# Kernel optimization log

Measured on AMD Instinct MI355X. Metric: run time of the kernel, lower is better.

The kernel has to match this reference:

```python
import jax, jax.numpy as jnp
import numpy as np

NUM_NODES = 50000
FEAT_DIM = 64
HIDDEN = 128
OUT_DIM = 128
NUM_EDGES = 640000


def setup_inputs() -> dict:
    key = jax.random.key(0)
    ks = jax.random.split(key, 8)
    edge_index = jax.random.randint(ks[0], (2, NUM_EDGES), 0, NUM_NODES, dtype=jnp.int32)
    emb = jax.random.normal(ks[1], (NUM_NODES, FEAT_DIM), dtype=jnp.float32) * 0.1
    # SAGEConv: lin_l (aggregated neighbors, with bias) and lin_r (root, no bias)
    s1 = 1.0 / np.sqrt(FEAT_DIM)
    W1l = jax.random.uniform(ks[2], (HIDDEN, FEAT_DIM), jnp.float32, -s1, s1)
    b1l = jnp.zeros((HIDDEN,), jnp.float32)
    W1r = jax.random.uniform(ks[3], (HIDDEN, FEAT_DIM), jnp.float32, -s1, s1)
    s2 = 1.0 / np.sqrt(HIDDEN)
    W2l = jax.random.uniform(ks[4], (OUT_DIM, HIDDEN), jnp.float32, -s2, s2)
    b2l = jnp.zeros((OUT_DIM,), jnp.float32)
    W2r = jax.random.uniform(ks[5], (OUT_DIM, HIDDEN), jnp.float32, -s2, s2)
    return {"edge_index": edge_index, "emb": emb, "W1l": W1l, "b1l": b1l,
            "W1r": W1r, "W2l": W2l, "b2l": b2l, "W2r": W2r}


def _sage_conv(x, src, dst, Wl, bl, Wr):
    # mean-aggregate source features at target nodes, then two linear paths
    msg = x[src]                                   # [E, d]
    agg = jax.ops.segment_sum(msg, dst, num_segments=NUM_NODES)
    deg = jax.ops.segment_sum(jnp.ones((src.shape[0],), x.dtype), dst,
                              num_segments=NUM_NODES)
    mean = agg / jnp.maximum(deg, 1.0)[:, None]    # [N, d]
    return mean @ Wl.T + bl + x @ Wr.T             # [N, out]


def reference(edge_index, emb, W1l, b1l, W1r, W2l, b2l, W2r):
    src, dst = edge_index[0], edge_index[1]
    h = jax.nn.relu(_sage_conv(emb, src, dst, W1l, b1l, W1r))
    return _sage_conv(h, src, dst, W2l, b2l, W2r)
```

## Files before the change

### kernel.cpp

```cpp
#include <hip/hip_runtime.h>

#define N_NODES 50000
#define FEAT    64
#define HID     128
#define N_EDGES 640000
#define NBLK    196
#define GCAP    64
#define SSTR    68

typedef __attribute__((ext_vector_type(8))) short bf16x8;
typedef __attribute__((ext_vector_type(4))) float f32x4;

static __device__ __forceinline__ unsigned short f2bf(float f) {
    unsigned u = __float_as_uint(f);
    u = u + 0x7fffu + ((u >> 16) & 1u);
    return (unsigned short)(u >> 16);
}
static __device__ __forceinline__ float bflo(unsigned u) {
    return __uint_as_float(u << 16);
}
static __device__ __forceinline__ float bfhi(unsigned u) {
    return __uint_as_float(u & 0xffff0000u);
}

static __device__ __forceinline__ void gridbar(int* bar, int gen) {
    __syncthreads();
    if (threadIdx.x == 0) {
        __threadfence();
        int arrived = atomicAdd(&bar[0], 1);
        if (arrived == NBLK - 1) {
            atomicExch(&bar[0], 0);
            __threadfence();
            atomicExch(&bar[1], gen);
        } else {
            while (atomicAdd(&bar[1], 0) < gen) __builtin_amdgcn_s_sleep(2);
        }
        __threadfence();
    }
    __syncthreads();
}

__global__ __launch_bounds__(256) void histcvt_kernel(
        const int* __restrict__ dst, const float* __restrict__ emb,
        const float* __restrict__ W1l, const float* __restrict__ W1r,
        const float* __restrict__ W2l, const float* __restrict__ W2r,
        int* __restrict__ count, int* __restrict__ eslot,
        unsigned* __restrict__ emb_bf_u, unsigned* __restrict__ Wbf_u) {
    int gtid = blockIdx.x * 256 + threadIdx.x;
    if (gtid < N_EDGES) {
        int slot = atomicAdd(&count[dst[gtid]], 1);
        eslot[gtid] = slot;
    }
    for (int i = gtid; i < N_NODES * FEAT / 2; i += N_EDGES) {
        float2 v = ((const float2*)emb)[i];
        emb_bf_u[i] = ((unsigned)f2bf(v.y) << 16) | (unsigned)f2bf(v.x);
    }
    if (gtid < 24576) {
        int w = gtid * 2;
        float lo, hi;
        if (w < 8192)       { lo = W1l[w];         hi = W1l[w + 1]; }
        else if (w < 16384) { lo = W1r[w - 8192];  hi = W1r[w - 8191]; }
        else if (w < 32768) { lo = W2l[w - 16384]; hi = W2l[w - 16383]; }
        else                { lo = W2r[w - 32768]; hi = W2r[w - 32767]; }
        Wbf_u[gtid] = ((unsigned)f2bf(hi) << 16) | (unsigned)f2bf(lo);
    }
}

__global__ __launch_bounds__(256) void scanperm_kernel(
        const int* __restrict__ count, int* offset, int* dhist, int* dcur,
        int* bsum, int* boff, int* dstart, int* perm, int* bar) {
    __shared__ int tmp[256];
    __shared__ int lh[64];
    __shared__ int lb2[64];
    int t = threadIdx.x;
    int gtid = blockIdx.x * 256 + t;

    {
        if (t < 64) lh[t] = 0;
        int v = (gtid < N_NODES) ? count[gtid] : 0;
        tmp[t] = v;
        __syncthreads();
        if (gtid < N_NODES) atomicAdd(&lh[v < 63 ? v : 63], 1);
        for (int off = 1; off < 256; off <<= 1) {
            int add = (t >= off) ? tmp[t - off] : 0;
            __syncthreads();
            tmp[t] += add;
            __syncthreads();
        }
        if (gtid < N_NODES) offset[gtid] = tmp[t] - v;
        if (t == 255) bsum[blockIdx.x] = tmp[255];
        if (t < 64 && lh[t] > 0) atomicAdd(&dhist[t], lh[t]);
    }
    gridbar(bar, 1);

    if (blockIdx.x < 2) {
        const int* in  = (blockIdx.x == 0) ? bsum : dhist;
        int*       out = (blockIdx.x == 0) ? boff : dstart;
        int cnt        = (blockIdx.x == 0) ? NBLK : 64;
        int v = (t < cnt) ? in[t] : 0;
        tmp[t] = v;
        __syncthreads();
        for (int off = 1; off < 256; off <<= 1) {
            int add = (t >= off) ? tmp[t - off] : 0;
            __syncthreads();
            tmp[t] += add;
            __syncthreads();
        }
        if (t < cnt) out[t] = tmp[t] - v;
    }
    gridbar(bar, 2);

    if (gtid < N_NODES) offset[gtid] += boff[blockIdx.x];
    if (gtid == 0) offset[N_NODES] = N_EDGES;
    {
        if (t < 64) lh[t] = 0;
        __syncthreads();
        int d = 0, slot = 0;
        if (gtid < N_NODES) {
            int c = count[gtid];
            d = c < 63 ? c : 63;
            slot = atomicAdd(&lh[d], 1);
        }
        __syncthreads();
        if (t < 64 && lh[t] > 0) lb2[t] = atomicAdd(&dcur[t], lh[t]);
        __syncthreads();
        if (gtid < N_NODES) perm[dstart[d] + lb2[d] + slot] = gtid;
    }
}

__global__ void fill_kernel(const int* __restrict__ src, const int* __restrict__ dst,
                            const int* __restrict__ offset,
                            const int* __restrict__ eslot, int* __restrict__ esrc) {
    int e = blockIdx.x * blockDim.x + threadIdx.x;
    if (e >= N_EDGES) return;
    esrc[offset[dst[e]] + eslot[e]] = src[e];
}

__global__ __launch_bounds__(256, 4) void fgemm1_kernel(
        const unsigned short* __restrict__ embb, const int* __restrict__ offset,
        const int* __restrict__ esrc, const int* __restrict__ perm,
        const short* __restrict__ Wl, const short* __restrict__ Wr,
        const float* __restrict__ bias, unsigned short* __restrict__ hout) {
    __shared__ unsigned short smean[16][72];
    __shared__ int sidx[16][SSTR];
    __shared__ int nid[16];
    int t = threadIdx.x;
    int bid = (int)gridDim.x - 1 - (int)blockIdx.x;
    if (t < 16) nid[t] = perm[bid * 16 + t];
    __syncthreads();

    int sub = t >> 4, fl = t & 15;
    int n = nid[sub];
    int beg = offset[n], deg = offset[n + 1] - beg;
    bool fast = deg <= GCAP;
    if (fast) { for (int j = fl; j < deg; j += 16) sidx[sub][j] = esrc[beg + j]; }
    float A0[4] = {0,0,0,0}, A1[4] = {0,0,0,0};
    const uint2* eb2 = (const uint2*)embb;
    #define ACC2(A, v) { \
        A[0]+=bflo((v).x); A[1]+=bfhi((v).x); A[2]+=bflo((v).y); A[3]+=bfhi((v).y); }
    {
        int i = 0;
        if (fast) {
            for (; i + 8 <= deg; i += 8) {
                int4 i0 = *(const int4*)&sidx[sub][i];
                int4 i1 = *(const int4*)&sidx[sub][i + 4];
                uint2 r0 = eb2[(size_t)i0.x * 16 + fl];
                uint2 r1 = eb2[(size_t)i0.y * 16 + fl];
                uint2 r2 = eb2[(size_t)i0.z * 16 + fl];
                uint2 r3 = eb2[(size_t)i0.w * 16 + fl];
                uint2 r4 = eb2[(size_t)i1.x * 16 + fl];
                uint2 r5 = eb2[(size_t)i1.y * 16 + fl];
                uint2 r6 = eb2[(size_t)i1.z * 16 + fl];
                uint2 r7 = eb2[(size_t)i1.w * 16 + fl];
                ACC2(A0, r0) ACC2(A1, r1) ACC2(A0, r2) ACC2(A1, r3)
                ACC2(A0, r4) ACC2(A1, r5) ACC2(A0, r6) ACC2(A1, r7)
            }
            for (; i + 4 <= deg; i += 4) {
                int4 i0 = *(const int4*)&sidx[sub][i];
                uint2 r0 = eb2[(size_t)i0.x * 16 + fl];
                uint2 r1 = eb2[(size_t)i0.y * 16 + fl];
                uint2 r2 = eb2[(size_t)i0.z * 16 + fl];
                uint2 r3 = eb2[(size_t)i0.w * 16 + fl];
                ACC2(A0, r0) ACC2(A1, r1) ACC2(A0, r2) ACC2(A1, r3)
            }
            for (; i < deg; ++i) {
                uint2 v = eb2[(size_t)sidx[sub][i] * 16 + fl];
                ACC2(A0, v)
            }
        } else {
            for (; i < deg; ++i) {
                uint2 v = eb2[(size_t)esrc[beg + i] * 16 + fl];
                ACC2(A0, v)
            }
        }
    }
    #undef ACC2
    float dinv = 1.0f / fmaxf((float)deg, 1.0f);
    float s0 = (A0[0] + A1[0]) * dinv;
    float s1 = (A0[1] + A1[1]) * dinv;
    float s2 = (A0[2] + A1[2]) * dinv;
    float s3 = (A0[3] + A1[3]) * dinv;
    uint2 o;
    o.x = ((unsigned)f2bf(s1) << 16) | (unsigned)f2bf(s0);
    o.y = ((unsigned)f2bf(s3) << 16) | (unsigned)f2bf(s2);
    *(uint2*)&smean[sub][fl * 4] = o;
    __syncthreads();

    int wave = t >> 6, lane = t & 63;
    int col = lane & 15, quad = lane >> 4;
    int ncol = nid[col];
    int nt0 = wave * 2, nt1 = nt0 + 1;
    f32x4 acc0 = (f32x4){0.f,0.f,0.f,0.f}, acc1 = (f32x4){0.f,0.f,0.f,0.f};
    #pragma unroll
    for (int kb = 0; kb < FEAT; kb += 32) {
        bf16x8 am = *(const bf16x8*)&smean[col][kb + quad * 8];
        bf16x8 ax = *(const bf16x8*)(embb + (size_t)ncol * FEAT + kb + quad * 8);
        bf16x8 bl0 = *(const bf16x8*)(Wl + (nt0 * 16 + col) * FEAT + kb + quad * 8);
        bf16x8 br0 = *(const bf16x8*)(Wr + (nt0 * 16 + col) * FEAT + kb + quad * 8);
        bf16x8 bl1 = *(const bf16x8*)(Wl + (nt1 * 16 + col) * FEAT + kb + quad * 8);
        bf16x8 br1 = *(const bf16x8*)(Wr + (nt1 * 16 + col) * FEAT + kb + quad * 8);
        acc0 = __builtin_amdgcn_mfma_f32_16x16x32_bf16(am, bl0, acc0, 0, 0, 0);
        acc0 = __builtin_amdgcn_mfma_f32_16x16x32_bf16(ax, br0, acc0, 0, 0, 0);
        acc1 = __builtin_amdgcn_mfma_f32_16x16x32_bf16(am, bl1, acc1, 0, 0, 0);
        acc1 = __builtin_amdgcn_mfma_f32_16x16x32_bf16(ax, br1, acc1, 0, 0, 0);
    }
    float bv0 = bias[nt0 * 16 + col];
    float bv1 = bias[nt1 * 16 + col];
    #pragma unroll
    for (int r = 0; r < 4; ++r) {
        int node = nid[quad * 4 + r];
        hout[(size_t)node * HID + nt0 * 16 + col] = f2bf(fmaxf(acc0[r] + bv0, 0.f));
        hout[(size_t)node * HID + nt1 * 16 + col] = f2bf(fmaxf(acc1[r] + bv1, 0.f));
    }
}

__global__ __launch_bounds__(256, 4) void fgemm2_kernel(
        const unsigned short* __restrict__ hbf, const int* __restrict__ offset,
        const int* __restrict__ esrc, const int* __restrict__ perm,
        const short* __restrict__ Wl, const short* __restrict__ Wr,
        const float* __restrict__ bias, float* __restrict__ out) {
    __shared__ unsigned short smean[16][136];
    __shared__ int sidx[16][SSTR];
    __shared__ int nid[16];
    int t = threadIdx.x;
    int bid = (int)gridDim.x - 1 - (int)blockIdx.x;
    if (t < 16) nid[t] = perm[bid * 16 + t];
    __syncthreads();

    int sub = t >> 4, fl = t & 15;
    int n = nid[sub];
    int beg = offset[n], deg = offset[n + 1] - beg;
    bool fast = deg <= GCAP;
    if (fast) { for (int j = fl; j < deg; j += 16) sidx[sub][j] = esrc[beg + j]; }
    float A0[8] = {0,0,0,0,0,0,0,0}, A1[8] = {0,0,0,0,0,0,0,0};
    const uint4* hb4 = (const uint4*)hbf;
    #define ACCU(A, v) { \
        A[0]+=bflo((v).x); A[1]+=bfhi((v).x); A[2]+=bflo((v).y); A[3]+=bfhi((v).y); \
        A[4]+=bflo((v).z); A[5]+=bfhi((v).z); A[6]+=bflo((v).w); A[7]+=bfhi((v).w); }
    {
        int i = 0;
        if (fast) {
            for (; i + 8 <= deg; i += 8) {
                int4 i0 = *(const int4*)&sidx[sub][i];
                int4 i1 = *(const int4*)&sidx[sub][i + 4];
                uint4 r0 = hb4[(size_t)i0.x * 16 + fl];
                uint4 r1 = hb4[(size_t)i0.y * 16 + fl];
                uint4 r2 = hb4[(size_t)i0.z * 16 + fl];
                uint4 r3 = hb4[(size_t)i0.w * 16 + fl];
                uint4 r4 = hb4[(size_t)i1.x * 16 + fl];
                uint4 r5 = hb4[(size_t)i1.y * 16 + fl];
                uint4 r6 = hb4[(size_t)i1.z * 16 + fl];
                uint4 r7 = hb4[(size_t)i1.w * 16 + fl];
                ACCU(A0, r0) ACCU(A1, r1) ACCU(A0, r2) ACCU(A1, r3)
                ACCU(A0, r4) ACCU(A1, r5) ACCU(A0, r6) ACCU(A1, r7)
            }
            for (; i + 4 <= deg; i += 4) {
                int4 i0 = *(const int4*)&sidx[sub][i];
                uint4 r0 = hb4[(size_t)i0.x * 16 + fl];
                uint4 r1 = hb4[(size_t)i0.y * 16 + fl];
                uint4 r2 = hb4[(size_t)i0.z * 16 + fl];
                uint4 r3 = hb4[(size_t)i0.w * 16 + fl];
                ACCU(A0, r0) ACCU(A1, r1) ACCU(A0, r2) ACCU(A1, r3)
            }
            for (; i < deg; ++i) {
                uint4 v = hb4[(size_t)sidx[sub][i] * 16 + fl];
                ACCU(A0, v)
            }
        } else {
            for (; i < deg; ++i) {
                uint4 v = hb4[(size_t)esrc[beg + i] * 16 + fl];
                ACCU(A0, v)
            }
        }
    }
    #undef ACCU
    float dinv = 1.0f / fmaxf((float)deg, 1.0f);
    unsigned ow[4];
    #pragma unroll
    for (int k = 0; k < 4; ++k) {
        float lo = (A0[2*k]   + A1[2*k])   * dinv;
        float hi = (A0[2*k+1] + A1[2*k+1]) * dinv;
        ow[k] = ((unsigned)f2bf(hi) << 16) | (unsigned)f2bf(lo);
    }
    uint4 o4 = {ow[0], ow[1], ow[2], ow[3]};
    *(uint4*)&smean[sub][fl * 8] = o4;
    __syncthreads();

    int wave = t >> 6, lane = t & 63;
    int col = lane & 15, quad = lane >> 4;
    int ncol = nid[col];
    int nt0 = wave * 2, nt1 = nt0 + 1;
    f32x4 acc0 = (f32x4){0.f,0.f,0.f,0.f}, acc1 = (f32x4){0.f,0.f,0.f,0.f};
    #pragma unroll
    for (int kb = 0; kb < HID; kb += 32) {
        bf16x8 am = *(const bf16x8*)&smean[col][kb + quad * 8];
        bf16x8 ax = *(const bf16x8*)(hbf + (size_t)ncol * HID + kb + quad * 8);
        bf16x8 bl0 = *(const bf16x8*)(Wl + (nt0 * 16 + col) * HID + kb + quad * 8);
        bf16x8 br0 = *(const bf16x8*)(Wr + (nt0 * 16 + col) * HID + kb + quad * 8);
        bf16x8 bl1 = *(const bf16x8*)(Wl + (nt1 * 16 + col) * HID + kb + quad * 8);
        bf16x8 br1 = *(const bf16x8*)(Wr + (nt1 * 16 + col) * HID + kb + quad * 8);
        acc0 = __builtin_amdgcn_mfma_f32_16x16x32_bf16(am, bl0, acc0, 0, 0, 0);
        acc0 = __builtin_amdgcn_mfma_f32_16x16x32_bf16(ax, br0, acc0, 0, 0, 0);
        acc1 = __builtin_amdgcn_mfma_f32_16x16x32_bf16(am, bl1, acc1, 0, 0, 0);
        acc1 = __builtin_amdgcn_mfma_f32_16x16x32_bf16(ax, br1, acc1, 0, 0, 0);
    }
    float bv0 = bias[nt0 * 16 + col];
    float bv1 = bias[nt1 * 16 + col];
    #pragma unroll
    for (int r = 0; r < 4; ++r) {
        int node = nid[quad * 4 + r];
        out[(size_t)node * HID + nt0 * 16 + col] = acc0[r] + bv0;
        out[(size_t)node * HID + nt1 * 16 + col] = acc1[r] + bv1;
    }
}

extern "C" void kernel_launch(void* const* d_in, const int* in_sizes, int n_in,
                              void* d_out, int out_size, void* d_ws, size_t ws_size,
                              hipStream_t stream) {
    const int*   edge_index = (const int*)d_in[0];
    const float* emb        = (const float*)d_in[1];
    const float* W1l        = (const float*)d_in[2];
    const float* b1l        = (const float*)d_in[3];
    const float* W1r        = (const float*)d_in[4];
    const float* W2l        = (const float*)d_in[5];
    const float* b2l        = (const float*)d_in[6];
    const float* W2r        = (const float*)d_in[7];
    float* out = (float*)d_out;

    const int* src = edge_index;
    const int* dst = edge_index + N_EDGES;

    int* iws    = (int*)d_ws;
    int* offset = iws;
    int* count  = iws + 50004;
    int* dhist  = iws + 100004;
    int* dcur   = iws + 100068;
    int* bar    = iws + 100132;
    int* bsum   = iws + 100136;
    int* boff   = iws + 100392;
    int* dstart = iws + 100648;
    int* perm   = iws + 100712;
    int* esrc   = iws + 150712;
    int* eslot  = iws + 790712;
    unsigned short* W1l_bf = (unsigned short*)(iws + 1430712);
    unsigned short* W1r_bf = (unsigned short*)(iws + 1434808);
    unsigned short* W2l_bf = (unsigned short*)(iws + 1438904);
    unsigned short* W2r_bf = (unsigned short*)(iws + 1447096);
    unsigned short* Wbf    = W1l_bf;
    unsigned short* emb_bf = (unsigned short*)(iws + 1455288);
    unsigned short* hbf    = (unsigned short*)(iws + 3055288);

    (void)hipMemsetAsync(count, 0, (size_t)(100136 - 50004) * sizeof(int), stream);

    histcvt_kernel<<<(N_EDGES + 255) / 256, 256, 0, stream>>>(
        dst, emb, W1l, W1r, W2l, W2r, count, eslot,
        (unsigned*)emb_bf, (unsigned*)Wbf);
    scanperm_kernel<<<NBLK, 256, 0, stream>>>(
        count, offset, dhist, dcur, bsum, boff, dstart, perm, bar);
    fill_kernel<<<(N_EDGES + 255) / 256, 256, 0, stream>>>(
        src, dst, offset, eslot, esrc);

    fgemm1_kernel<<<N_NODES / 16, 256, 0, stream>>>(
        emb_bf, offset, esrc, perm,
        (const short*)W1l_bf, (const short*)W1r_bf, b1l, hbf);
    fgemm2_kernel<<<N_NODES / 16, 256, 0, stream>>>(
        hbf, offset, esrc, perm,
        (const short*)W2l_bf, (const short*)W2r_bf, b2l, out);
}
```

Baseline: 233.8 us.

## Fuse preprocessing kernels into one persistent kernel with grid barriers

Merges the memset, histogram/convert, scan/permutation and CSR fill kernels into a single persistent kernel of 1024 blocks that uses software grid barriers between phases. Counts are zeroed inside the kernel and only the barrier words are memset. The goal is to remove several kernel launches and their gaps. In exchange it adds five grid-wide barriers, and it relies on all 1024 blocks being co-resident to avoid deadlock.

```diff
diff --git a/kernel.cpp b/kernel.cpp
--- a/kernel.cpp
+++ b/kernel.cpp
@@ -4,7 +4,9 @@
 #define FEAT    64
 #define HID     128
 #define N_EDGES 640000
-#define NBLK    196
+#define PBLK    1024
+#define PGSZ    (PBLK * 256)
+#define SCANB   196
 #define GCAP    64
 #define SSTR    68
 
@@ -28,7 +30,7 @@
     if (threadIdx.x == 0) {
         __threadfence();
         int arrived = atomicAdd(&bar[0], 1);
-        if (arrived == NBLK - 1) {
+        if (arrived == PBLK - 1) {
             atomicExch(&bar[0], 0);
             __threadfence();
             atomicExch(&bar[1], gen);
@@ -40,18 +42,23 @@
     __syncthreads();
 }
 
-__global__ __launch_bounds__(256) void histcvt_kernel(
-        const int* __restrict__ dst, const float* __restrict__ emb,
+__global__ __launch_bounds__(256, 8) void prep_kernel(
+        const int* __restrict__ src, const int* __restrict__ dst,
+        const float* __restrict__ emb,
         const float* __restrict__ W1l, const float* __restrict__ W1r,
         const float* __restrict__ W2l, const float* __restrict__ W2r,
-        int* __restrict__ count, int* __restrict__ eslot,
-        unsigned* __restrict__ emb_bf_u, unsigned* __restrict__ Wbf_u) {
-    int gtid = blockIdx.x * 256 + threadIdx.x;
-    if (gtid < N_EDGES) {
-        int slot = atomicAdd(&count[dst[gtid]], 1);
-        eslot[gtid] = slot;
-    }
-    for (int i = gtid; i < N_NODES * FEAT / 2; i += N_EDGES) {
+        int* count, int* offset, int* dhist, int* dcur,
+        int* bsum, int* boff, int* dstart, int* perm,
+        int* esrc, int* eslot,
+        unsigned* emb_bf_u, unsigned* Wbf_u, int* bar) {
+    __shared__ int tmp[256];
+    __shared__ int lh[64];
+    __shared__ int lb2[64];
+    int t = threadIdx.x;
+    int gtid = blockIdx.x * 256 + t;
+
+    for (int i = gtid; i < 50128; i += PGSZ) count[i] = 0;
+    for (int i = gtid; i < N_NODES * FEAT / 2; i += PGSZ) {
         float2 v = ((const float2*)emb)[i];
         emb_bf_u[i] = ((unsigned)f2bf(v.y) << 16) | (unsigned)f2bf(v.x);
     }
@@ -64,18 +71,15 @@
         else                { lo = W2r[w - 32768]; hi = W2r[w - 32767]; }
         Wbf_u[gtid] = ((unsigned)f2bf(hi) << 16) | (unsigned)f2bf(lo);
     }
-}
-
-__global__ __launch_bounds__(256) void scanperm_kernel(
-        const int* __restrict__ count, int* offset, int* dhist, int* dcur,
-        int* bsum, int* boff, int* dstart, int* perm, int* bar) {
-    __shared__ int tmp[256];
-    __shared__ int lh[64];
-    __shared__ int lb2[64];
-    int t = threadIdx.x;
-    int gtid = blockIdx.x * 256 + t;
-
-    {
+    gridbar(bar, 1);
+
+    for (int e = gtid; e < N_EDGES; e += PGSZ) {
+        int slot = atomicAdd(&count[dst[e]], 1);
+        eslot[e] = slot;
+    }
+    gridbar(bar, 2);
+
+    if (blockIdx.x < SCANB) {
         if (t < 64) lh[t] = 0;
         int v = (gtid < N_NODES) ? count[gtid] : 0;
         tmp[t] = v;
@@ -91,12 +95,12 @@
         if (t == 255) bsum[blockIdx.x] = tmp[255];
         if (t < 64 && lh[t] > 0) atomicAdd(&dhist[t], lh[t]);
     }
-    gridbar(bar, 1);
+    gridbar(bar, 3);
 
     if (blockIdx.x < 2) {
         const int* in  = (blockIdx.x == 0) ? bsum : dhist;
         int*       out = (blockIdx.x == 0) ? boff : dstart;
-        int cnt        = (blockIdx.x == 0) ? NBLK : 64;
+        int cnt        = (blockIdx.x == 0) ? SCANB : 64;
         int v = (t < cnt) ? in[t] : 0;
         tmp[t] = v;
         __syncthreads();
@@ -108,11 +112,11 @@
         }
         if (t < cnt) out[t] = tmp[t] - v;
     }
-    gridbar(bar, 2);
-
-    if (gtid < N_NODES) offset[gtid] += boff[blockIdx.x];
-    if (gtid == 0) offset[N_NODES] = N_EDGES;
-    {
+    gridbar(bar, 4);
+
+    if (blockIdx.x < SCANB) {
+        if (gtid < N_NODES) offset[gtid] += boff[blockIdx.x];
+        if (gtid == 0) offset[N_NODES] = N_EDGES;
         if (t < 64) lh[t] = 0;
         __syncthreads();
         int d = 0, slot = 0;
@@ -126,14 +130,11 @@
         __syncthreads();
         if (gtid < N_NODES) perm[dstart[d] + lb2[d] + slot] = gtid;
     }
-}
-
-__global__ void fill_kernel(const int* __restrict__ src, const int* __restrict__ dst,
-                            const int* __restrict__ offset,
-                            const int* __restrict__ eslot, int* __restrict__ esrc) {
-    int e = blockIdx.x * blockDim.x + threadIdx.x;
-    if (e >= N_EDGES) return;
-    esrc[offset[dst[e]] + eslot[e]] = src[e];
+    gridbar(bar, 5);
+
+    for (int e = gtid; e < N_EDGES; e += PGSZ) {
+        esrc[offset[dst[e]] + eslot[e]] = src[e];
+    }
 }
 
 __global__ __launch_bounds__(256, 4) void fgemm1_kernel(
@@ -370,15 +371,12 @@
     unsigned short* emb_bf = (unsigned short*)(iws + 1455288);
     unsigned short* hbf    = (unsigned short*)(iws + 3055288);
 
-    (void)hipMemsetAsync(count, 0, (size_t)(100136 - 50004) * sizeof(int), stream);
-
-    histcvt_kernel<<<(N_EDGES + 255) / 256, 256, 0, stream>>>(
-        dst, emb, W1l, W1r, W2l, W2r, count, eslot,
-        (unsigned*)emb_bf, (unsigned*)Wbf);
-    scanperm_kernel<<<NBLK, 256, 0, stream>>>(
-        count, offset, dhist, dcur, bsum, boff, dstart, perm, bar);
-    fill_kernel<<<(N_EDGES + 255) / 256, 256, 0, stream>>>(
-        src, dst, offset, eslot, esrc);
+    (void)hipMemsetAsync(bar, 0, 16, stream);
+
+    prep_kernel<<<PBLK, 256, 0, stream>>>(
+        src, dst, emb, W1l, W1r, W2l, W2r,
+        count, offset, dhist, dcur, bsum, boff, dstart, perm, esrc, eslot,
+        (unsigned*)emb_bf, (unsigned*)Wbf, bar);
 
     fgemm1_kernel<<<N_NODES / 16, 256, 0, stream>>>(
         emb_bf, offset, esrc, perm,
```

Result: slower. 552.7 us (+136.4%).
